# Kernel optimization log

Hardware: AMD Instinct MI355X
Metric: run time of the kernel (lower is better)

Reference implementation:

```python
import jax, jax.numpy as jnp
import numpy as np

NEG_INF = -1e9
HIDDEN = 1024
HEADS = 16
SPH = HIDDEN // HEADS  # 64
B, Q, M = 8, 512, 512
R = Q + M


def rel_shift(x):
    # x: [N, H, Q, R] -> TransformerXL relative shift
    N, H, Qd, Rd = x.shape
    x = jnp.pad(x, ((0, 0), (0, 0), (0, 0), (1, 0)))
    x = x.reshape(N, H, Rd + 1, Qd)
    return x[:, :, 1:, :].reshape(N, H, Qd, Rd)


def setup_inputs() -> dict:
    key = jax.random.key(0)
    ks = jax.random.split(key, 11)
    std = 1.0 / np.sqrt(HIDDEN)
    # causal token mask: query position i (global pos M+i) may attend to ref pos j <= M+i
    q_pos = jnp.arange(Q)[:, None] + M
    r_pos = jnp.arange(R)[None, :]
    token_mask = (r_pos > q_pos).astype(jnp.float32)[None, None]  # [1,1,Q,R]
    return {
        "query_seqs": jax.random.normal(ks[0], (B, Q, HIDDEN), jnp.float32),
        "memory_seqs": jax.random.normal(ks[1], (B, M, HIDDEN), jnp.float32),
        "positional_encoding": jax.random.normal(ks[2], (R, HIDDEN), jnp.float32),
        "token_mask": token_mask,
        "content_bias": jax.random.normal(ks[3], (HEADS, SPH), jnp.float32) * 0.02,
        "position_bias": jax.random.normal(ks[4], (HEADS, SPH), jnp.float32) * 0.02,
        "Wq": jax.random.normal(ks[5], (HIDDEN, HEADS, SPH), jnp.float32) * std,
        "Wkc": jax.random.normal(ks[6], (HIDDEN, HEADS, SPH), jnp.float32) * std,
        "Wkp": jax.random.normal(ks[7], (HIDDEN, HEADS, SPH), jnp.float32) * std,
        "Wv": jax.random.normal(ks[8], (HIDDEN, HEADS, SPH), jnp.float32) * std,
        "Wo": jax.random.normal(ks[9], (HEADS, SPH, HIDDEN), jnp.float32) * std,
    }


def reference(query_seqs, memory_seqs, positional_encoding, token_mask,
              content_bias, position_bias, Wq, Wkc, Wkp, Wv, Wo):
    reference_seqs = jnp.concatenate([memory_seqs, query_seqs], axis=1)  # [B,R,D]
    query = jnp.einsum('nqd,dhs->nqhs', query_seqs, Wq)            # [B,Q,H,S]
    key_content = jnp.einsum('nrd,dhs->nrhs', reference_seqs, Wkc)  # [B,R,H,S]
    key_position = jnp.einsum('rd,dhs->rhs', positional_encoding, Wkp)  # [R,H,S]
    value = jnp.einsum('nrd,dhs->nrhs', reference_seqs, Wv)         # [B,R,H,S]

    content = jnp.einsum('nqhs,nrhs->nhqr', query + content_bias, key_content)
    positions = jnp.einsum('nqhs,rhs->nhqr', query + position_bias, key_position)
    positions = rel_shift(positions)

    scores = (content + positions) / np.sqrt(SPH) + token_mask * NEG_INF
    attn = jax.nn.softmax(scores, axis=3)  # [B,H,Q,R]
    out = jnp.einsum('nhqr,nrhs->nqhs', attn, value)
    return jnp.einsum('nqhs,hsd->nqd', out, Wo)  # [B,Q,D]
```

## Files before the change

### kernel.cpp

```cpp
#include <hip/hip_runtime.h>

#define B_ 8
#define Q_ 512
#define M_ 512
#define R_ 1024
#define H_ 16
#define S_ 64
#define D_ 1024
#define MEG 1048576L

typedef unsigned short ushort_t;
typedef __attribute__((ext_vector_type(8))) _Float16 f16x8;
typedef __attribute__((ext_vector_type(8))) unsigned short u16x8;
typedef __attribute__((ext_vector_type(4))) float f32x4;
typedef __attribute__((ext_vector_type(2))) unsigned int u32x2;

__device__ __forceinline__ unsigned short h2u(_Float16 h) {
    union { _Float16 h; unsigned short u; } v; v.h = h; return v.u;
}
__device__ __forceinline__ unsigned int pk_f16(float a, float b) {
    union { _Float16 h[2]; unsigned int u; } v;
    v.h[0] = (_Float16)a; v.h[1] = (_Float16)b; return v.u;
}
__device__ __forceinline__ void async_cp16(const ushort_t* g, ushort_t* l) {
    __builtin_amdgcn_global_load_lds(
        (const __attribute__((address_space(1))) void*)g,
        (__attribute__((address_space(3))) void*)l, 16, 0, 0);
}

__global__ __launch_bounds__(256) void zero_out_f32_k(float* __restrict__ p, int n) {
    int i = blockIdx.x * 256 + threadIdx.x;
    if (i < n) p[i] = 0.f;
}

__global__ __launch_bounds__(256) void conv_bias_k(const float* __restrict__ cb,
                                                   const float* __restrict__ pb,
                                                   ushort_t* __restrict__ outb) {
    int i = blockIdx.x * 256 + threadIdx.x;
    if (i < 1024) {
        outb[i]        = h2u((_Float16)cb[i]);
        outb[1024 + i] = h2u((_Float16)pb[i]);
    }
}

__global__ __launch_bounds__(256) void cvt_all_k(const float* __restrict__ mem,
                                                 const float* __restrict__ qry,
                                                 const float* __restrict__ pos,
                                                 ushort_t* __restrict__ qcat,
                                                 ushort_t* __restrict__ posb) {
    int r = blockIdx.x, g = blockIdx.y;
    const float* src;
    ushort_t* dst;
    if (g < 8) {
        src = (r < 512) ? (mem + ((long)g * 512 + r) * 1024)
                        : (qry + ((long)g * 512 + (r - 512)) * 1024);
        dst = qcat + ((long)g * 1024 + r) * 1024;
    } else {
        src = pos + (long)r * 1024;
        dst = posb + (long)r * 1024;
    }
    int i = threadIdx.x * 4;
    f32x4 v = *(const f32x4*)(src + i);
    u32x2 o; o[0] = pk_f16(v[0], v[1]); o[1] = pk_f16(v[2], v[3]);
    *(u32x2*)(dst + i) = o;
}

__global__ __launch_bounds__(256) void transW_k(
    const float* __restrict__ w0, const float* __restrict__ w1,
    const float* __restrict__ w2, const float* __restrict__ w3,
    const float* __restrict__ w4,
    ushort_t* __restrict__ d0, ushort_t* __restrict__ d1,
    ushort_t* __restrict__ d2, ushort_t* __restrict__ d3,
    ushort_t* __restrict__ d4) {
    const float* in; ushort_t* out;
    switch (blockIdx.z) {
        case 0: in = w0; out = d0; break;
        case 1: in = w1; out = d1; break;
        case 2: in = w2; out = d2; break;
        case 3: in = w3; out = d3; break;
        default: in = w4; out = d4; break;
    }
    __shared__ ushort_t tile[32][33];
    int bx = blockIdx.x * 32, by = blockIdx.y * 32;
    int tx = threadIdx.x, ty = threadIdx.y;
    #pragma unroll
    for (int i = 0; i < 32; i += 8)
        tile[ty + i][tx] = h2u((_Float16)in[(long)(by + ty + i) * 1024 + bx + tx]);
    __syncthreads();
    #pragma unroll
    for (int i = 0; i < 32; i += 8)
        out[(long)(bx + ty + i) * 1024 + by + tx] = tile[tx][ty + i];
}

__global__ __launch_bounds__(256) void trans_v_k(const ushort_t* __restrict__ bigC,
                                                 ushort_t* __restrict__ vT) {
    int rt = blockIdx.x, h = blockIdx.y, b = blockIdx.z;
    __shared__ __align__(16) ushort_t tile[64][72];
    int t = threadIdx.x, row = t >> 2, c0 = (t & 3) * 16;
    const ushort_t* src = bigC + ((long)(b * R_ + rt * 64 + row)) * 2048 + 1024 + h * 64;
    *(u16x8*)&tile[row][c0]     = *(const u16x8*)(src + c0);
    *(u16x8*)&tile[row][c0 + 8] = *(const u16x8*)(src + c0 + 8);
    __syncthreads();
    ushort_t* dst = vT + ((long)(b * 1024 + h * 64 + row)) * 1024 + rt * 64;
    u16x8 o0, o1;
    #pragma unroll
    for (int i = 0; i < 8; ++i) { o0[i] = tile[c0 + i][row]; o1[i] = tile[c0 + 8 + i][row]; }
    *(u16x8*)(dst + c0)     = o0;
    *(u16x8*)(dst + c0 + 8) = o1;
}

__device__ __forceinline__ void gemm_body(const ushort_t* Arow0,
                                          const ushort_t* BTrow0,
                                          void* Crow0, long crs, int out_f32) {
    __shared__ __align__(16) ushort_t Al[128 * 32];
    __shared__ __align__(16) ushort_t Bl[128 * 32];

    int t = threadIdx.x;
    int wave = t >> 6, lane = t & 63, quad = lane >> 4, l16 = lane & 15;
    int wm = (wave & 1) * 64, wn = (wave >> 1) * 64;

    f32x4 acc[4][4];
    #pragma unroll
    for (int im = 0; im < 4; ++im)
        #pragma unroll
        for (int in = 0; in < 4; ++in) acc[im][in] = (f32x4){0.f, 0.f, 0.f, 0.f};

    int grow = lane >> 2, gcol = (lane & 3) * 8;
    const ushort_t* ga0 = Arow0 + (long)(wave * 32 + grow) * 1024 + gcol;
    const ushort_t* ga1 = Arow0 + (long)(wave * 32 + 16 + grow) * 1024 + gcol;
    const ushort_t* gb0 = BTrow0 + (long)(wave * 32 + grow) * 1024 + gcol;
    const ushort_t* gb1 = BTrow0 + (long)(wave * 32 + 16 + grow) * 1024 + gcol;
    ushort_t* la0 = &Al[(wave * 2 + 0) * 512];
    ushort_t* la1 = &Al[(wave * 2 + 1) * 512];
    ushort_t* lb0 = &Bl[(wave * 2 + 0) * 512];
    ushort_t* lb1 = &Bl[(wave * 2 + 1) * 512];

    for (int k0 = 0; k0 < 1024; k0 += 32) {
        __syncthreads();
        async_cp16(ga0 + k0, la0);
        async_cp16(ga1 + k0, la1);
        async_cp16(gb0 + k0, lb0);
        async_cp16(gb1 + k0, lb1);
        __syncthreads();

        f16x8 af[4], bf[4];
        #pragma unroll
        for (int im = 0; im < 4; ++im)
            af[im] = *(const f16x8*)&Al[(wm + im * 16 + l16) * 32 + quad * 8];
        #pragma unroll
        for (int in = 0; in < 4; ++in)
            bf[in] = *(const f16x8*)&Bl[(wn + in * 16 + l16) * 32 + quad * 8];
        #pragma unroll
        for (int im = 0; im < 4; ++im)
            #pragma unroll
            for (int in = 0; in < 4; ++in)
                acc[im][in] = __builtin_amdgcn_mfma_f32_16x16x32_f16(
                    af[im], bf[in], acc[im][in], 0, 0, 0);
    }

    #pragma unroll
    for (int im = 0; im < 4; ++im)
        #pragma unroll
        for (int in = 0; in < 4; ++in)
            #pragma unroll
            for (int reg = 0; reg < 4; ++reg) {
                long addr = (long)(wm + im * 16 + quad * 4 + reg) * crs
                          + wn + in * 16 + l16;
                if (out_f32) ((float*)Crow0)[addr] = acc[im][in][reg];
                else ((ushort_t*)Crow0)[addr] = h2u((_Float16)acc[im][in][reg]);
            }
}

__global__ __launch_bounds__(256) void gemm_mega(
    const ushort_t* __restrict__ qcat, const ushort_t* __restrict__ posb,
    const ushort_t* __restrict__ BT4,
    ushort_t* __restrict__ bigC, ushort_t* __restrict__ qproj,
    ushort_t* __restrict__ kpp) {
    int z = blockIdx.z, x = blockIdx.x, y = blockIdx.y;
    const ushort_t* Arow0;
    const ushort_t* BTrow0;
    ushort_t* Crow0;
    long crs;
    if (z < 8) {
        Arow0  = qcat + (long)z * MEG + (long)x * 128 * 1024;
        BTrow0 = BT4 + (long)y * 128 * 1024;
        Crow0  = bigC + (long)z * 2 * MEG + (long)x * 128 * 2048 + y * 128;
        crs = 2048;
    } else if (z == 8) {
        if (y >= 8) return;
        Arow0  = posb + (long)x * 128 * 1024;
        BTrow0 = BT4 + (long)(2048 + y * 128) * 1024;
        Crow0  = kpp + (long)x * 128 * 1024 + y * 128;
        crs = 1024;
    } else {
        if (x >= 4 || y >= 8) return;
        int b = z - 9;
        Arow0  = qcat + (long)b * MEG + (long)(512 + x * 128) * 1024;
        BTrow0 = BT4 + (long)(3072 + y * 128) * 1024;
        Crow0  = qproj + (long)b * 512 * 1024 + (long)x * 128 * 1024 + y * 128;
        crs = 1024;
    }
    gemm_body(Arow0, BTrow0, Crow0, crs, 0);
}

__global__ __launch_bounds__(256) void gemm_fin(
    const ushort_t* __restrict__ A, const ushort_t* __restrict__ WoT,
    float* __restrict__ out) {
    gemm_body(A + (long)blockIdx.x * 128 * 1024,
              WoT + (long)blockIdx.y * 128 * 1024,
              out + (long)blockIdx.x * 128 * 1024 + blockIdx.y * 128, 1024, 1);
}

__global__ __launch_bounds__(512) void attn_kernel(
    const ushort_t* __restrict__ qproj,
    const ushort_t* __restrict__ kc,
    const ushort_t* __restrict__ kp,
    const ushort_t* __restrict__ vT,
    const ushort_t* __restrict__ cbpb,
    ushort_t* __restrict__ aout)
{
    int qt = (blockIdx.x + ((blockIdx.y >> 6) << 1)) & 3;
    int q0 = qt * 128;
    int bh = blockIdx.y;
    int b = bh >> 4, h = bh & 15;
    int t = threadIdx.x;
    int wave = t >> 6, lane = t & 63, quad = lane >> 4, l16 = lane & 15;

    __shared__ __align__(16) ushort_t Kc[64][72];
    __shared__ __align__(16) ushort_t Vt[64][72];
    __shared__ __align__(16) ushort_t Kp[192][72];
    __shared__ __align__(16) char DPu[8][2816];
    _Float16* Dl = (_Float16*)&DPu[wave][0];
    ushort_t* Pl = (ushort_t*)&DPu[wave][0];

    const ushort_t* qrow = qproj + ((long)(b * Q_ + q0 + wave * 16 + l16)) * 1024 + h * 64;
    f16x8 qcf[2], qpf[2];
    #pragma unroll
    for (int ks = 0; ks < 2; ++ks) {
        f16x8 qv  = *(const f16x8*)(qrow + ks * 32 + quad * 8);
        f16x8 cbv = *(const f16x8*)(cbpb + h * 64 + ks * 32 + quad * 8);
        f16x8 pbv = *(const f16x8*)(cbpb + 1024 + h * 64 + ks * 32 + quad * 8);
        qcf[ks] = qv + cbv;
        qpf[ks] = qv + pbv;
    }

    float m_s[4], l_s[4];
    f32x4 o_acc[4];
    #pragma unroll
    for (int r = 0; r < 4; ++r) {
        m_s[r] = -1e30f; l_s[r] = 0.f;
        o_acc[r] = (f32x4){0.f, 0.f, 0.f, 0.f};
    }

    int srow = t >> 3, sc0 = (t & 7) * 8;
    const ushort_t* kcb = kc + ((long)(b * R_) + srow) * 2048 + h * 64 + sc0;
    const ushort_t* vtb = vT + ((long)(b * 1024 + h * 64 + srow)) * 1024 + sc0;
    const ushort_t* kpb = kp + h * 64 + sc0;

    int ntiles = ((q0 + 639) >> 6) + 1;

    u16x8 rKc = *(const u16x8*)(kcb);
    u16x8 rVt = *(const u16x8*)(vtb);
    u16x8 rKp[3];
    {
        int jb0 = 384 - q0;
        #pragma unroll
        for (int p = 0; p < 3; ++p) {
            int j = jb0 + p * 64 + srow;
            int jc = j > 1023 ? 1023 : j;
            rKp[p] = *(const u16x8*)(kpb + (long)jc * 1024);
        }
    }

    for (int it = 0; it < ntiles; ++it) {
        int r0 = it * 64;
        int jbase = r0 - q0 + 384;
        int gb0 = jbase >> 4;
        __syncthreads();
        *(u16x8*)&Kc[srow][sc0] = rKc;
        *(u16x8*)&Vt[srow][sc0] = rVt;
        if (it == 0) {
            #pragma unroll
            for (int p = 0; p < 3; ++p) {
                int j = jbase + p * 64 + srow;
                int ph = ((j >> 4) % 12) * 16 + (j & 15);
                *(u16x8*)&Kp[ph][sc0] = rKp[p];
            }
        } else {
            int j = jbase + 128 + srow;
            int ph = ((j >> 4) % 12) * 16 + (j & 15);
            *(u16x8*)&Kp[ph][sc0] = rKp[0];
        }
        __syncthreads();
        if (it + 1 < ntiles) {
            int r1 = r0 + 64;
            rKc = *(const u16x8*)(kcb + (long)r1 * 2048);
            rVt = *(const u16x8*)(vtb + r1);
            int j = r1 - q0 + 512 + srow;
            int jc = j > 1023 ? 1023 : j;
            rKp[0] = *(const u16x8*)(kpb + (long)jc * 1024);
        }

        f32x4 sc[4];
        #pragma unroll
        for (int s = 0; s < 4; ++s) sc[s] = (f32x4){0.f, 0.f, 0.f, 0.f};
        #pragma unroll
        for (int ks = 0; ks < 2; ++ks)
            #pragma unroll
            for (int sub = 0; sub < 4; ++sub) {
                f16x8 bb = *(const f16x8*)&Kc[sub * 16 + l16][ks * 32 + quad * 8];
                sc[sub] = __builtin_amdgcn_mfma_f32_16x16x32_f16(qcf[ks], bb, sc[sub], 0, 0, 0);
            }

        f32x4 dd[5];
        #pragma unroll
        for (int s = 0; s < 5; ++s) dd[s] = (f32x4){0.f, 0.f, 0.f, 0.f};
        #pragma unroll
        for (int ks = 0; ks < 2; ++ks)
            #pragma unroll
            for (int sub = 0; sub < 5; ++sub) {
                int pb = (gb0 + 7 - wave + sub) % 12;
                f16x8 bb = *(const f16x8*)&Kp[pb * 16 + l16][ks * 32 + quad * 8];
                dd[sub] = __builtin_amdgcn_mfma_f32_16x16x32_f16(qpf[ks], bb, dd[sub], 0, 0, 0);
            }
        #pragma unroll
        for (int sub = 0; sub < 5; ++sub)
            #pragma unroll
            for (int reg = 0; reg < 4; ++reg)
                Dl[(quad * 4 + reg) * 88 + sub * 16 + l16] = (_Float16)dd[sub][reg];

        #pragma unroll
        for (int sub = 0; sub < 4; ++sub) {
            int rl = sub * 16 + l16;
            #pragma unroll
            for (int reg = 0; reg < 4; ++reg) {
                int row16 = quad * 4 + reg;
                float dval = (float)Dl[row16 * 88 + rl - row16 + 15];
                float sv = (sc[sub][reg] + dval) * 0.125f;
                if (r0 + rl > q0 + wave * 16 + row16 + 512) sv = -1e30f;
                sc[sub][reg] = sv;
            }
        }

        float rm[4];
        #pragma unroll
        for (int reg = 0; reg < 4; ++reg) {
            float v = fmaxf(fmaxf(sc[0][reg], sc[1][reg]), fmaxf(sc[2][reg], sc[3][reg]));
            #pragma unroll
            for (int m = 1; m < 16; m <<= 1) v = fmaxf(v, __shfl_xor(v, m));
            rm[reg] = v;
        }
        float alpha[4];
        #pragma unroll
        for (int reg = 0; reg < 4; ++reg) {
            float mn = fmaxf(m_s[reg], rm[reg]);
            alpha[reg] = __expf(m_s[reg] - mn);
            m_s[reg] = mn;
        }
        float rs[4] = {0.f, 0.f, 0.f, 0.f};
        #pragma unroll
        for (int sub = 0; sub < 4; ++sub)
            #pragma unroll
            for (int reg = 0; reg < 4; ++reg) {
                float p = __expf(sc[sub][reg] - m_s[reg]);
                rs[reg] += p;
                Pl[(quad * 4 + reg) * 72 + sub * 16 + l16] = h2u((_Float16)p);
            }
        #pragma unroll
        for (int reg = 0; reg < 4; ++reg) {
            float v = rs[reg];
            #pragma unroll
            for (int m = 1; m < 16; m <<= 1) v += __shfl_xor(v, m);
            l_s[reg] = l_s[reg] * alpha[reg] + v;
        }
        #pragma unroll
        for (int sub = 0; sub < 4; ++sub)
            #pragma unroll
            for (int reg = 0; reg < 4; ++reg)
                o_acc[sub][reg] *= alpha[reg];

        #pragma unroll
        for (int ks = 0; ks < 2; ++ks) {
            f16x8 a = *(const f16x8*)&Pl[l16 * 72 + ks * 32 + quad * 8];
            #pragma unroll
            for (int sub = 0; sub < 4; ++sub) {
                f16x8 bb = *(const f16x8*)&Vt[sub * 16 + l16][ks * 32 + quad * 8];
                o_acc[sub] = __builtin_amdgcn_mfma_f32_16x16x32_f16(a, bb, o_acc[sub], 0, 0, 0);
            }
        }
    }

    #pragma unroll
    for (int reg = 0; reg < 4; ++reg) {
        float inv = 1.f / l_s[reg];
        int qg = q0 + wave * 16 + quad * 4 + reg;
        ushort_t* orow = aout + ((long)(b * Q_ + qg)) * 1024 + h * 64;
        #pragma unroll
        for (int sub = 0; sub < 4; ++sub)
            orow[sub * 16 + l16] = h2u((_Float16)(o_acc[sub][reg] * inv));
    }
}

extern "C" void kernel_launch(void* const* d_in, const int* in_sizes, int n_in,
                              void* d_out, int out_size, void* d_ws, size_t ws_size,
                              hipStream_t stream) {
    const float* query  = (const float*)d_in[0];
    const float* memory = (const float*)d_in[1];
    const float* pos    = (const float*)d_in[2];
    const float* cb  = (const float*)d_in[4];
    const float* pb  = (const float*)d_in[5];
    const float* Wq  = (const float*)d_in[6];
    const float* Wkc = (const float*)d_in[7];
    const float* Wkp = (const float*)d_in[8];
    const float* Wv  = (const float*)d_in[9];
    const float* Wo  = (const float*)d_in[10];
    float* out = (float*)d_out;
    ushort_t* ws = (ushort_t*)d_ws;

    size_t ws_elems = ws_size / 2;
    if (ws_elems < 36 * MEG) {
        zero_out_f32_k<<<(out_size + 255) / 256, 256, 0, stream>>>(out, out_size);
        return;
    }

    ushort_t* cbpb  = ws;
    ushort_t* BT4   = ws + MEG;
    ushort_t* WoT   = BT4 + 4 * MEG;
    ushort_t* kpp   = WoT + MEG;
    ushort_t* posb  = kpp + MEG;
    ushort_t* qproj = posb + MEG;
    ushort_t* bigC  = qproj + 4 * MEG;
    ushort_t* qcat  = bigC + 16 * MEG;
    ushort_t* vTb   = qcat;
    ushort_t* aout  = qproj;

    conv_bias_k<<<4, 256, 0, stream>>>(cb, pb, cbpb);
    transW_k<<<dim3(32, 32, 5), dim3(32, 8), 0, stream>>>(
        Wkc, Wv, Wkp, Wq, Wo,
        BT4, BT4 + MEG, BT4 + 2 * MEG, BT4 + 3 * MEG, WoT);
    cvt_all_k<<<dim3(1024, 9), 256, 0, stream>>>(memory, query, pos, qcat, posb);

    gemm_mega<<<dim3(8, 16, 17), 256, 0, stream>>>(qcat, posb, BT4, bigC, qproj, kpp);
    trans_v_k<<<dim3(16, 16, 8), 256, 0, stream>>>(bigC, vTb);
    attn_kernel<<<dim3(4, 128), 512, 0, stream>>>(qproj, bigC, kpp, vTb, cbpb, aout);
    gemm_fin<<<dim3(32, 8, 1), 256, 0, stream>>>(aout, WoT, out);
}
```

Baseline: 300.1 us.

## Fuse prep kernels, write V transposed from GEMM, register-prefetch GEMM loads

Merges the bias conversion, weight transpose and input conversion kernels into one prep launch. The projection GEMM now writes V directly in transposed layout, which removes the separate transpose kernel and its extra pass over V. The GEMM mainloop replaces async global-to-LDS copies with register-staged prefetch of the next K tile. The combined effect is fewer launches and less memory traffic, but the register prefetch may raise register pressure and the transposed store is less coalesced.

```diff
diff --git a/kernel.cpp b/kernel.cpp
--- a/kernel.cpp
+++ b/kernel.cpp
@@ -12,6 +12,7 @@
 typedef unsigned short ushort_t;
 typedef __attribute__((ext_vector_type(8))) _Float16 f16x8;
 typedef __attribute__((ext_vector_type(8))) unsigned short u16x8;
+typedef __attribute__((ext_vector_type(4))) unsigned short u16x4;
 typedef __attribute__((ext_vector_type(4))) float f32x4;
 typedef __attribute__((ext_vector_type(2))) unsigned int u32x2;
 
@@ -22,96 +23,69 @@
     union { _Float16 h[2]; unsigned int u; } v;
     v.h[0] = (_Float16)a; v.h[1] = (_Float16)b; return v.u;
 }
-__device__ __forceinline__ void async_cp16(const ushort_t* g, ushort_t* l) {
-    __builtin_amdgcn_global_load_lds(
-        (const __attribute__((address_space(1))) void*)g,
-        (__attribute__((address_space(3))) void*)l, 16, 0, 0);
-}
 
 __global__ __launch_bounds__(256) void zero_out_f32_k(float* __restrict__ p, int n) {
     int i = blockIdx.x * 256 + threadIdx.x;
     if (i < n) p[i] = 0.f;
 }
 
-__global__ __launch_bounds__(256) void conv_bias_k(const float* __restrict__ cb,
-                                                   const float* __restrict__ pb,
-                                                   ushort_t* __restrict__ outb) {
-    int i = blockIdx.x * 256 + threadIdx.x;
-    if (i < 1024) {
-        outb[i]        = h2u((_Float16)cb[i]);
-        outb[1024 + i] = h2u((_Float16)pb[i]);
-    }
-}
-
-__global__ __launch_bounds__(256) void cvt_all_k(const float* __restrict__ mem,
-                                                 const float* __restrict__ qry,
-                                                 const float* __restrict__ pos,
-                                                 ushort_t* __restrict__ qcat,
-                                                 ushort_t* __restrict__ posb) {
-    int r = blockIdx.x, g = blockIdx.y;
-    const float* src;
-    ushort_t* dst;
-    if (g < 8) {
-        src = (r < 512) ? (mem + ((long)g * 512 + r) * 1024)
-                        : (qry + ((long)g * 512 + (r - 512)) * 1024);
-        dst = qcat + ((long)g * 1024 + r) * 1024;
+__global__ __launch_bounds__(256) void prep_k(
+    const float* __restrict__ mem, const float* __restrict__ qry,
+    const float* __restrict__ pos, const float* __restrict__ cb,
+    const float* __restrict__ pb,
+    const float* __restrict__ Wkc, const float* __restrict__ Wv,
+    const float* __restrict__ Wkp, const float* __restrict__ Wq,
+    const float* __restrict__ Wo,
+    ushort_t* __restrict__ qcat, ushort_t* __restrict__ posb,
+    ushort_t* __restrict__ cbpb, ushort_t* __restrict__ BT4,
+    ushort_t* __restrict__ WoT) {
+    int x = blockIdx.x, y = blockIdx.y, t = threadIdx.x;
+    if (y < 5) {
+        const float* in; ushort_t* out;
+        switch (y) {
+            case 0: in = Wkc; out = BT4;           break;
+            case 1: in = Wv;  out = BT4 + MEG;     break;
+            case 2: in = Wkp; out = BT4 + 2 * MEG; break;
+            case 3: in = Wq;  out = BT4 + 3 * MEG; break;
+            default: in = Wo; out = WoT;           break;
+        }
+        __shared__ ushort_t tile[32][33];
+        int bx = (x & 31) * 32, by = (x >> 5) * 32;
+        int tx = t & 31, ty = t >> 5;
+        #pragma unroll
+        for (int i = 0; i < 32; i += 8)
+            tile[ty + i][tx] = h2u((_Float16)in[(long)(by + ty + i) * 1024 + bx + tx]);
+        __syncthreads();
+        #pragma unroll
+        for (int i = 0; i < 32; i += 8)
+            out[(long)(bx + ty + i) * 1024 + by + tx] = tile[tx][ty + i];
+    } else if (y < 13) {
+        int g = y - 5, r = x;
+        const float* src = (r < 512) ? (mem + ((long)g * 512 + r) * 1024)
+                                     : (qry + ((long)g * 512 + (r - 512)) * 1024);
+        ushort_t* dst = qcat + ((long)g * 1024 + r) * 1024;
+        int i = t * 4;
+        f32x4 v = *(const f32x4*)(src + i);
+        u32x2 o; o[0] = pk_f16(v[0], v[1]); o[1] = pk_f16(v[2], v[3]);
+        *(u32x2*)(dst + i) = o;
+    } else if (y == 13) {
+        int i = t * 4;
+        f32x4 v = *(const f32x4*)(pos + (long)x * 1024 + i);
+        u32x2 o; o[0] = pk_f16(v[0], v[1]); o[1] = pk_f16(v[2], v[3]);
+        *(u32x2*)(posb + (long)x * 1024 + i) = o;
     } else {
-        src = pos + (long)r * 1024;
-        dst = posb + (long)r * 1024;
-    }
-    int i = threadIdx.x * 4;
-    f32x4 v = *(const f32x4*)(src + i);
-    u32x2 o; o[0] = pk_f16(v[0], v[1]); o[1] = pk_f16(v[2], v[3]);
-    *(u32x2*)(dst + i) = o;
-}
-
-__global__ __launch_bounds__(256) void transW_k(
-    const float* __restrict__ w0, const float* __restrict__ w1,
-    const float* __restrict__ w2, const float* __restrict__ w3,
-    const float* __restrict__ w4,
-    ushort_t* __restrict__ d0, ushort_t* __restrict__ d1,
-    ushort_t* __restrict__ d2, ushort_t* __restrict__ d3,
-    ushort_t* __restrict__ d4) {
-    const float* in; ushort_t* out;
-    switch (blockIdx.z) {
-        case 0: in = w0; out = d0; break;
-        case 1: in = w1; out = d1; break;
-        case 2: in = w2; out = d2; break;
-        case 3: in = w3; out = d3; break;
-        default: in = w4; out = d4; break;
-    }
-    __shared__ ushort_t tile[32][33];
-    int bx = blockIdx.x * 32, by = blockIdx.y * 32;
-    int tx = threadIdx.x, ty = threadIdx.y;
-    #pragma unroll
-    for (int i = 0; i < 32; i += 8)
-        tile[ty + i][tx] = h2u((_Float16)in[(long)(by + ty + i) * 1024 + bx + tx]);
-    __syncthreads();
-    #pragma unroll
-    for (int i = 0; i < 32; i += 8)
-        out[(long)(bx + ty + i) * 1024 + by + tx] = tile[tx][ty + i];
-}
-
-__global__ __launch_bounds__(256) void trans_v_k(const ushort_t* __restrict__ bigC,
-                                                 ushort_t* __restrict__ vT) {
-    int rt = blockIdx.x, h = blockIdx.y, b = blockIdx.z;
-    __shared__ __align__(16) ushort_t tile[64][72];
-    int t = threadIdx.x, row = t >> 2, c0 = (t & 3) * 16;
-    const ushort_t* src = bigC + ((long)(b * R_ + rt * 64 + row)) * 2048 + 1024 + h * 64;
-    *(u16x8*)&tile[row][c0]     = *(const u16x8*)(src + c0);
-    *(u16x8*)&tile[row][c0 + 8] = *(const u16x8*)(src + c0 + 8);
-    __syncthreads();
-    ushort_t* dst = vT + ((long)(b * 1024 + h * 64 + row)) * 1024 + rt * 64;
-    u16x8 o0, o1;
-    #pragma unroll
-    for (int i = 0; i < 8; ++i) { o0[i] = tile[c0 + i][row]; o1[i] = tile[c0 + 8 + i][row]; }
-    *(u16x8*)(dst + c0)     = o0;
-    *(u16x8*)(dst + c0 + 8) = o1;
+        if (x == 0) {
+            for (int i = t; i < 1024; i += 256) {
+                cbpb[i]        = h2u((_Float16)cb[i]);
+                cbpb[1024 + i] = h2u((_Float16)pb[i]);
+            }
+        }
+    }
 }
 
 __device__ __forceinline__ void gemm_body(const ushort_t* Arow0,
                                           const ushort_t* BTrow0,
-                                          void* Crow0, long crs, int out_f32) {
+                                          void* Crow0, long crs, int mode) {
     __shared__ __align__(16) ushort_t Al[128 * 32];
     __shared__ __align__(16) ushort_t Bl[128 * 32];
 
@@ -125,23 +99,30 @@
         #pragma unroll
         for (int in = 0; in < 4; ++in) acc[im][in] = (f32x4){0.f, 0.f, 0.f, 0.f};
 
-    int grow = lane >> 2, gcol = (lane & 3) * 8;
-    const ushort_t* ga0 = Arow0 + (long)(wave * 32 + grow) * 1024 + gcol;
-    const ushort_t* ga1 = Arow0 + (long)(wave * 32 + 16 + grow) * 1024 + gcol;
-    const ushort_t* gb0 = BTrow0 + (long)(wave * 32 + grow) * 1024 + gcol;
-    const ushort_t* gb1 = BTrow0 + (long)(wave * 32 + 16 + grow) * 1024 + gcol;
-    ushort_t* la0 = &Al[(wave * 2 + 0) * 512];
-    ushort_t* la1 = &Al[(wave * 2 + 1) * 512];
-    ushort_t* lb0 = &Bl[(wave * 2 + 0) * 512];
-    ushort_t* lb1 = &Bl[(wave * 2 + 1) * 512];
+    int srow = t >> 1, sseg = (t & 1) * 16;
+    const ushort_t* ga = Arow0 + (long)srow * 1024 + sseg;
+    const ushort_t* gb = BTrow0 + (long)srow * 1024 + sseg;
+    ushort_t* la = &Al[srow * 32 + sseg];
+    ushort_t* lb = &Bl[srow * 32 + sseg];
+
+    u16x8 rA0 = *(const u16x8*)(ga);
+    u16x8 rA1 = *(const u16x8*)(ga + 8);
+    u16x8 rB0 = *(const u16x8*)(gb);
+    u16x8 rB1 = *(const u16x8*)(gb + 8);
 
     for (int k0 = 0; k0 < 1024; k0 += 32) {
         __syncthreads();
-        async_cp16(ga0 + k0, la0);
-        async_cp16(ga1 + k0, la1);
-        async_cp16(gb0 + k0, lb0);
-        async_cp16(gb1 + k0, lb1);
+        *(u16x8*)la       = rA0;
+        *(u16x8*)(la + 8) = rA1;
+        *(u16x8*)lb       = rB0;
+        *(u16x8*)(lb + 8) = rB1;
         __syncthreads();
+        if (k0 + 32 < 1024) {
+            rA0 = *(const u16x8*)(ga + k0 + 32);
+            rA1 = *(const u16x8*)(ga + k0 + 40);
+            rB0 = *(const u16x8*)(gb + k0 + 32);
+            rB1 = *(const u16x8*)(gb + k0 + 40);
+        }
 
         f16x8 af[4], bf[4];
         #pragma unroll
@@ -158,6 +139,19 @@
                     af[im], bf[in], acc[im][in], 0, 0, 0);
     }
 
+    if (mode == 2) {
+        #pragma unroll
+        for (int im = 0; im < 4; ++im)
+            #pragma unroll
+            for (int in = 0; in < 4; ++in) {
+                u16x4 pk;
+                #pragma unroll
+                for (int reg = 0; reg < 4; ++reg) pk[reg] = h2u((_Float16)acc[im][in][reg]);
+                long addr = (long)(wn + in * 16 + l16) * 1024 + wm + im * 16 + quad * 4;
+                *(u16x4*)((ushort_t*)Crow0 + addr) = pk;
+            }
+        return;
+    }
     #pragma unroll
     for (int im = 0; im < 4; ++im)
         #pragma unroll
@@ -166,7 +160,7 @@
             for (int reg = 0; reg < 4; ++reg) {
                 long addr = (long)(wm + im * 16 + quad * 4 + reg) * crs
                           + wn + in * 16 + l16;
-                if (out_f32) ((float*)Crow0)[addr] = acc[im][in][reg];
+                if (mode == 1) ((float*)Crow0)[addr] = acc[im][in][reg];
                 else ((ushort_t*)Crow0)[addr] = h2u((_Float16)acc[im][in][reg]);
             }
 }
@@ -174,33 +168,31 @@
 __global__ __launch_bounds__(256) void gemm_mega(
     const ushort_t* __restrict__ qcat, const ushort_t* __restrict__ posb,
     const ushort_t* __restrict__ BT4,
-    ushort_t* __restrict__ bigC, ushort_t* __restrict__ qproj,
-    ushort_t* __restrict__ kpp) {
+    ushort_t* __restrict__ kcC, ushort_t* __restrict__ vT,
+    ushort_t* __restrict__ qproj, ushort_t* __restrict__ kpp) {
     int z = blockIdx.z, x = blockIdx.x, y = blockIdx.y;
-    const ushort_t* Arow0;
-    const ushort_t* BTrow0;
-    ushort_t* Crow0;
-    long crs;
     if (z < 8) {
-        Arow0  = qcat + (long)z * MEG + (long)x * 128 * 1024;
-        BTrow0 = BT4 + (long)y * 128 * 1024;
-        Crow0  = bigC + (long)z * 2 * MEG + (long)x * 128 * 2048 + y * 128;
-        crs = 2048;
+        const ushort_t* Arow0 = qcat + (long)z * MEG + (long)x * 128 * 1024;
+        if (y < 8) {
+            gemm_body(Arow0, BT4 + (long)y * 128 * 1024,
+                      kcC + (long)z * MEG + (long)x * 128 * 1024 + y * 128, 1024, 0);
+        } else {
+            int n0 = (y - 8) * 128;
+            gemm_body(Arow0, BT4 + (long)(1024 + n0) * 1024,
+                      vT + ((long)z * 1024 + n0) * 1024 + x * 128, 0, 2);
+        }
     } else if (z == 8) {
         if (y >= 8) return;
-        Arow0  = posb + (long)x * 128 * 1024;
-        BTrow0 = BT4 + (long)(2048 + y * 128) * 1024;
-        Crow0  = kpp + (long)x * 128 * 1024 + y * 128;
-        crs = 1024;
+        gemm_body(posb + (long)x * 128 * 1024,
+                  BT4 + (long)(2048 + y * 128) * 1024,
+                  kpp + (long)x * 128 * 1024 + y * 128, 1024, 0);
     } else {
         if (x >= 4 || y >= 8) return;
         int b = z - 9;
-        Arow0  = qcat + (long)b * MEG + (long)(512 + x * 128) * 1024;
-        BTrow0 = BT4 + (long)(3072 + y * 128) * 1024;
-        Crow0  = qproj + (long)b * 512 * 1024 + (long)x * 128 * 1024 + y * 128;
-        crs = 1024;
-    }
-    gemm_body(Arow0, BTrow0, Crow0, crs, 0);
+        gemm_body(qcat + (long)b * MEG + (long)(512 + x * 128) * 1024,
+                  BT4 + (long)(3072 + y * 128) * 1024,
+                  qproj + (long)b * 512 * 1024 + (long)x * 128 * 1024 + y * 128, 1024, 0);
+    }
 }
 
 __global__ __launch_bounds__(256) void gemm_fin(
@@ -253,7 +245,7 @@
     }
 
     int srow = t >> 3, sc0 = (t & 7) * 8;
-    const ushort_t* kcb = kc + ((long)(b * R_) + srow) * 2048 + h * 64 + sc0;
+    const ushort_t* kcb = kc + ((long)(b * R_) + srow) * 1024 + h * 64 + sc0;
     const ushort_t* vtb = vT + ((long)(b * 1024 + h * 64 + srow)) * 1024 + sc0;
     const ushort_t* kpb = kp + h * 64 + sc0;
 
@@ -294,7 +286,7 @@
         __syncthreads();
         if (it + 1 < ntiles) {
             int r1 = r0 + 64;
-            rKc = *(const u16x8*)(kcb + (long)r1 * 2048);
+            rKc = *(const u16x8*)(kcb + (long)r1 * 1024);
             rVt = *(const u16x8*)(vtb + r1);
             int j = r1 - q0 + 512 + srow;
             int jc = j > 1023 ? 1023 : j;
@@ -429,19 +421,15 @@
     ushort_t* kpp   = WoT + MEG;
     ushort_t* posb  = kpp + MEG;
     ushort_t* qproj = posb + MEG;
-    ushort_t* bigC  = qproj + 4 * MEG;
-    ushort_t* qcat  = bigC + 16 * MEG;
-    ushort_t* vTb   = qcat;
+    ushort_t* kcC   = qproj + 4 * MEG;
+    ushort_t* vT    = kcC + 8 * MEG;
+    ushort_t* qcat  = vT + 8 * MEG;
     ushort_t* aout  = qproj;
 
-    conv_bias_k<<<4, 256, 0, stream>>>(cb, pb, cbpb);
-    transW_k<<<dim3(32, 32, 5), dim3(32, 8), 0, stream>>>(
-        Wkc, Wv, Wkp, Wq, Wo,
-        BT4, BT4 + MEG, BT4 + 2 * MEG, BT4 + 3 * MEG, WoT);
-    cvt_all_k<<<dim3(1024, 9), 256, 0, stream>>>(memory, query, pos, qcat, posb);
-
-    gemm_mega<<<dim3(8, 16, 17), 256, 0, stream>>>(qcat, posb, BT4, bigC, qproj, kpp);
-    trans_v_k<<<dim3(16, 16, 8), 256, 0, stream>>>(bigC, vTb);
-    attn_kernel<<<dim3(4, 128), 512, 0, stream>>>(qproj, bigC, kpp, vTb, cbpb, aout);
+    prep_k<<<dim3(1024, 15), 256, 0, stream>>>(
+        memory, query, pos, cb, pb, Wkc, Wv, Wkp, Wq, Wo,
+        qcat, posb, cbpb, BT4, WoT);
+    gemm_mega<<<dim3(8, 16, 17), 256, 0, stream>>>(qcat, posb, BT4, kcC, vT, qproj, kpp);
+    attn_kernel<<<dim3(4, 128), 512, 0, stream>>>(qproj, kcC, kpp, vT, cbpb, aout);
     gemm_fin<<<dim3(32, 8, 1), 256, 0, stream>>>(aout, WoT, out);
 }
```

Result: faster. 293.1 us (-2.3%).
